# Optimization experiments

Hardware: AMD Instinct MI355X
Metric: run time of the kernel (lower is better)

The kernel has to match this reference:

```python
import jax, jax.numpy as jnp
import numpy as np

B, T, D, H = 16384, 48, 32, 64  # batch, num_lags, input_dim(num_features), hidden_size


def setup_inputs() -> dict:
    key = jax.random.key(0)
    ks = jax.random.split(key, 8)
    s = 1.0 / np.sqrt(H)  # torch-style uniform bound magnitude, approximated via scaled normal
    return {
        "x": jax.random.normal(ks[0], (B, T, D), dtype=jnp.float32),
        "h0": jax.random.normal(ks[1], (B, H), dtype=jnp.float32) * 0.01,
        "c0": jax.random.normal(ks[2], (B, H), dtype=jnp.float32) * 0.01,
        "W_att": jax.random.normal(ks[3], (1, 2 * H + T), dtype=jnp.float32) * 0.05,
        "b_att": jnp.zeros((1,), dtype=jnp.float32),
        "W_ih": jax.random.normal(ks[4], (4 * H, D), dtype=jnp.float32) * s,
        "W_hh": jax.random.normal(ks[5], (4 * H, H), dtype=jnp.float32) * s,
        "b_ih": jnp.zeros((4 * H,), dtype=jnp.float32),
        "b_hh": jnp.zeros((4 * H,), dtype=jnp.float32),
    }


def reference(x, h0, c0, W_att, b_att, W_ih, W_hh, b_ih, b_hh):
    # x: [B, T, D];  input-attention DA-RNN encoder with single-layer LSTM.
    Bn, Tn, Dn = x.shape
    Hn = h0.shape[-1]
    xT = jnp.transpose(x, (0, 2, 1))  # [B, D, T] full per-feature series, constant over t
    w_att = W_att[0]                   # [2H+T]

    def step(carry, xt):
        ht, ct = carry  # [B, H]
        hrep = jnp.broadcast_to(ht[:, None, :], (Bn, Dn, Hn))
        crep = jnp.broadcast_to(ct[:, None, :], (Bn, Dn, Hn))
        feat = jnp.concatenate([hrep, crep, xT], axis=2)  # [B, D, 2H+T]
        et = jnp.einsum('bdf,f->bd', feat, w_att) + b_att[0]  # [B, D]
        at = jax.nn.softmax(et, axis=1)                        # softmax over features
        wi = at * xt                                           # [B, D]
        gates = wi @ W_ih.T + b_ih + ht @ W_hh.T + b_hh        # [B, 4H]
        i_g, f_g, g_g, o_g = jnp.split(gates, 4, axis=1)
        i_g = jax.nn.sigmoid(i_g)
        f_g = jax.nn.sigmoid(f_g)
        g_g = jnp.tanh(g_g)
        o_g = jax.nn.sigmoid(o_g)
        ct2 = f_g * ct + i_g * g_g
        ht2 = o_g * jnp.tanh(ct2)
        return (ht2, ct2), (at, ht2)

    xs = jnp.transpose(x, (1, 0, 2))  # [T, B, D]
    _, (ats, hts) = jax.lax.scan(step, (h0, c0), xs)
    attention = jnp.transpose(ats, (1, 0, 2))       # [B, T, D]
    input_encoded = jnp.transpose(hts, (1, 0, 2))   # [B, T, H]
    return attention, input_encoded
```

## Files before the change

kernel.cpp:

```cpp
#include <hip/hip_runtime.h>

#define TT 48
#define DD 32
#define HH 64
#define BB 16384
#define LOG2E 1.4426950408889634f

typedef __bf16 bf16x8 __attribute__((ext_vector_type(8)));
typedef float f32x4 __attribute__((ext_vector_type(4)));

#define MFMA(a, b, c) __builtin_amdgcn_mfma_f32_16x16x32_bf16(a, b, c, 0, 0, 0)
#define BC(v) __builtin_bit_cast(bf16x8, v)

static __device__ __forceinline__ float exp2_f(float v) {
#if __has_builtin(__builtin_amdgcn_exp2f)
  return __builtin_amdgcn_exp2f(v);
#else
  return exp2f(v);
#endif
}
static __device__ __forceinline__ unsigned short bfu(float f) {
  __bf16 b = (__bf16)f;
  return __builtin_bit_cast(unsigned short, b);
}
static __device__ __forceinline__ float sigm2(float y) {
  return __builtin_amdgcn_rcpf(1.f + exp2_f(-y));
}
static __device__ __forceinline__ float tanh2(float y) {
  return fmaf(-2.f, __builtin_amdgcn_rcpf(1.f + exp2_f(y)), 1.f);
}


__global__ void prep_kernel(const float* __restrict__ W_ih, const float* __restrict__ W_hh,
                            const float* __restrict__ b_ih, const float* __restrict__ b_hh,
                            unsigned short* __restrict__ WhhL, unsigned short* __restrict__ WihL,
                            float* __restrict__ bsumL) {
  const int tid = threadIdx.x;
  const int l = tid & 63, qt = tid >> 6;
  const int rowl = l & 15, kq = (l >> 4) * 8;
  for (int mm = 0; mm < 4; ++mm) {
    const int m = qt * 4 + mm;
    const int g = m >> 2, hq = m & 3;
    const float s = (g == 2) ? 2.f * LOG2E : LOG2E;
    const int hidx = (hq >> 1) * 32 + (rowl >> 2) * 8 + (hq & 1) * 4 + (rowl & 3);
    const int orig = g * 64 + hidx;
    for (int c = 0; c < 2; ++c)
      for (int j = 0; j < 8; ++j)
        WhhL[(m * 2 + c) * 512 + l * 8 + j] = bfu(W_hh[orig * 64 + c * 32 + kq + j] * s);
    for (int j = 0; j < 8; ++j)
      WihL[m * 512 + l * 8 + j] = bfu(W_ih[orig * 32 + kq + j] * s);
    if ((l >> 4) == 0) bsumL[m * 16 + rowl] = (b_ih[orig] + b_hh[orig]) * s;
  }
}

static __device__ __forceinline__ void lstm_step(
    const int t, const float* __restrict__ xp, float* __restrict__ o0,
    float* __restrict__ opq, const float* av, float* xv,
    const f32x4 (&whhHi)[16][2], const f32x4 (&wihR)[16], const f32x4 (&biasR)[16],
    f32x4 (&creg)[4], bf16x8 (&bhIn)[2], bf16x8 (&bhOut)[2],
    const float4 av0, const float4 av1) {
  *(float4*)(o0 + t * DD) = av0;
  *(float4*)(o0 + t * DD + 4) = av1;
  bf16x8 bxw;
#pragma unroll
  for (int j = 0; j < 8; ++j) bxw[j] = (__bf16)(xv[j] * av[j]);
  const int tn = (t + 2 < TT) ? (t + 2) : (TT - 1);
  {
    const float* xnp = xp + (size_t)tn * DD;
    float4 x0 = *(const float4*)xnp, x1 = *(const float4*)(xnp + 4);
    xv[0] = x0.x; xv[1] = x0.y; xv[2] = x0.z; xv[3] = x0.w;
    xv[4] = x1.x; xv[5] = x1.y; xv[6] = x1.z; xv[7] = x1.w;
  }
#pragma unroll
  for (int hq = 0; hq < 4; ++hq) {
    f32x4 acc[4];
#pragma unroll
    for (int g = 0; g < 4; ++g) {
      const int m = g * 4 + hq;
      f32x4 A = MFMA(BC(wihR[m]), bxw, biasR[m]);
      A = MFMA(BC(whhHi[m][0]), bhIn[0], A);
      A = MFMA(BC(whhHi[m][1]), bhIn[1], A);
      acc[g] = A;
    }
    float hr[4];
#pragma unroll
    for (int r = 0; r < 4; ++r) {
      float ig = sigm2(acc[0][r]);
      float fg = sigm2(acc[1][r]);
      float gts = fmaf(-4.f * LOG2E,
                       __builtin_amdgcn_rcpf(1.f + exp2_f(acc[2][r])), 2.f * LOG2E);
      float og = sigm2(acc[3][r]);
      float cns = fmaf(fg, creg[hq][r], ig * gts);
      creg[hq][r] = cns;
      hr[r] = og * tanh2(cns);
    }
    float4 hv;
    hv.x = hr[0]; hv.y = hr[1]; hv.z = hr[2]; hv.w = hr[3];
    *(float4*)(opq + (size_t)t * HH + (hq >> 1) * 32 + (hq & 1) * 4) = hv;
#pragma unroll
    for (int r = 0; r < 4; ++r) bhOut[hq >> 1][(hq & 1) * 4 + r] = (__bf16)hr[r];
  }
}

__global__ __launch_bounds__(256, 1) void lstm_kernel(
    const float* __restrict__ x, const float* __restrict__ h0, const float* __restrict__ c0,
    const float* __restrict__ W_att, const unsigned short* __restrict__ WhhL,
    const unsigned short* __restrict__ WihL, const float* __restrict__ bsumL,
    float* __restrict__ out0, float* __restrict__ out1) {
  const int tid = threadIdx.x;
  const int l = tid & 63;
  const int wid = tid >> 6;
  const int b = l & 15;
  const int qp = l >> 4;
  const int brow = blockIdx.x * 64 + wid * 16 + b;

  f32x4 whhHi[16][2], wihR[16], biasR[16];
#pragma unroll
  for (int m = 0; m < 16; ++m) {
#pragma unroll
    for (int c = 0; c < 2; ++c)
      whhHi[m][c] = *(const f32x4*)(WhhL + ((m * 2 + c) << 9) + l * 8);
    wihR[m] = *(const f32x4*)(WihL + (m << 9) + l * 8);
    biasR[m] = *(const f32x4*)(bsumL + m * 16 + qp * 4);
  }
#pragma unroll
  for (int m = 0; m < 16; ++m) {
#pragma unroll
    for (int c = 0; c < 2; ++c) asm volatile("" : "+v"(whhHi[m][c]));
    asm volatile("" : "+a"(wihR[m]));
    asm volatile("" : "+a"(biasR[m]));
  }

  const float* xp = x + (size_t)brow * (TT * DD) + qp * 8;

  float p[8];
#pragma unroll
  for (int j = 0; j < 8; ++j) p[j] = 0.f;
#pragma unroll 4
  for (int t = 0; t < TT; ++t) {
    const float w = W_att[2 * HH + t];
    float4 x0 = *(const float4*)(xp + t * DD);
    float4 x1 = *(const float4*)(xp + t * DD + 4);
    p[0] = fmaf(x0.x, w, p[0]); p[1] = fmaf(x0.y, w, p[1]);
    p[2] = fmaf(x0.z, w, p[2]); p[3] = fmaf(x0.w, w, p[3]);
    p[4] = fmaf(x1.x, w, p[4]); p[5] = fmaf(x1.y, w, p[5]);
    p[6] = fmaf(x1.z, w, p[6]); p[7] = fmaf(x1.w, w, p[7]);
  }
  float av[8];
  {
    float mx = fmaxf(fmaxf(fmaxf(p[0], p[1]), fmaxf(p[2], p[3])),
                     fmaxf(fmaxf(p[4], p[5]), fmaxf(p[6], p[7])));
    mx = fmaxf(mx, __shfl_xor(mx, 16));
    mx = fmaxf(mx, __shfl_xor(mx, 32));
    float s = 0.f;
#pragma unroll
    for (int j = 0; j < 8; ++j) {
      av[j] = exp2_f((p[j] - mx) * LOG2E);
      s += av[j];
    }
    s += __shfl_xor(s, 16);
    s += __shfl_xor(s, 32);
    float inv = __builtin_amdgcn_rcpf(s);
#pragma unroll
    for (int j = 0; j < 8; ++j) av[j] *= inv;
  }
  float4 av0, av1;
  av0.x = av[0]; av0.y = av[1]; av0.z = av[2]; av0.w = av[3];
  av1.x = av[4]; av1.y = av[5]; av1.z = av[6]; av1.w = av[7];
  float* o0 = out0 + (size_t)brow * (TT * DD) + qp * 8;

  f32x4 creg[4];
#pragma unroll
  for (int hq = 0; hq < 4; ++hq) {
    f32x4 cv = *(const f32x4*)(c0 + (size_t)brow * HH + (hq >> 1) * 32 + qp * 8 + (hq & 1) * 4);
#pragma unroll
    for (int r = 0; r < 4; ++r) cv[r] *= 2.f * LOG2E;
    creg[hq] = cv;
  }

  bf16x8 bhA[2], bhB[2];
#pragma unroll
  for (int c = 0; c < 2; ++c) {
    const float* hp = h0 + (size_t)brow * HH + c * 32 + qp * 8;
    float4 v0 = *(const float4*)hp, v1 = *(const float4*)(hp + 4);
    float vv[8] = {v0.x, v0.y, v0.z, v0.w, v1.x, v1.y, v1.z, v1.w};
#pragma unroll
    for (int j = 0; j < 8; ++j) bhA[c][j] = (__bf16)vv[j];
  }

  float* opq = out1 + (size_t)brow * (TT * HH) + qp * 8;
  float xvA[8], xvB[8];
  {
    float4 x0 = *(const float4*)xp, x1 = *(const float4*)(xp + 4);
    xvA[0] = x0.x; xvA[1] = x0.y; xvA[2] = x0.z; xvA[3] = x0.w;
    xvA[4] = x1.x; xvA[5] = x1.y; xvA[6] = x1.z; xvA[7] = x1.w;
    float4 y0 = *(const float4*)(xp + DD), y1 = *(const float4*)(xp + DD + 4);
    xvB[0] = y0.x; xvB[1] = y0.y; xvB[2] = y0.z; xvB[3] = y0.w;
    xvB[4] = y1.x; xvB[5] = y1.y; xvB[6] = y1.z; xvB[7] = y1.w;
  }

#pragma unroll 1
  for (int t = 0; t < TT; t += 2) {
    lstm_step(t, xp, o0, opq, av, xvA, whhHi, wihR, biasR, creg, bhA, bhB, av0, av1);
    lstm_step(t + 1, xp, o0, opq, av, xvB, whhHi, wihR, biasR, creg, bhB, bhA, av0, av1);
  }
}

extern "C" void kernel_launch(void* const* d_in, const int* in_sizes, int n_in,
                              void* d_out, int out_size, void* d_ws, size_t ws_size,
                              hipStream_t stream) {
  const float* x = (const float*)d_in[0];
  const float* h0 = (const float*)d_in[1];
  const float* c0 = (const float*)d_in[2];
  const float* W_att = (const float*)d_in[3];
  const float* W_ih = (const float*)d_in[5];
  const float* W_hh = (const float*)d_in[6];
  const float* b_ih = (const float*)d_in[7];
  const float* b_hh = (const float*)d_in[8];

  float* out0 = (float*)d_out;
  float* out1 = out0 + (size_t)BB * TT * DD;

  char* ws = (char*)d_ws;
  unsigned short* WhhL = (unsigned short*)ws;
  unsigned short* WihL = (unsigned short*)(ws + 32768);
  float* bsumL = (float*)(ws + 49152);

  prep_kernel<<<1, 256, 0, stream>>>(W_ih, W_hh, b_ih, b_hh, WhhL, WihL, bsumL);
  lstm_kernel<<<BB / 64, 256, 0, stream>>>(x, h0, c0, W_att, WhhL, WihL, bsumL, out0, out1);
}
```

Before: 120.1 us.

## Interleave two independent batch tiles per wave to hide recurrence latency

```diff
diff --git a/kernel.cpp b/kernel.cpp
--- a/kernel.cpp
+++ b/kernel.cpp
@@ -102,37 +102,9 @@
   }
 }
 
-__global__ __launch_bounds__(256, 1) void lstm_kernel(
-    const float* __restrict__ x, const float* __restrict__ h0, const float* __restrict__ c0,
-    const float* __restrict__ W_att, const unsigned short* __restrict__ WhhL,
-    const unsigned short* __restrict__ WihL, const float* __restrict__ bsumL,
-    float* __restrict__ out0, float* __restrict__ out1) {
-  const int tid = threadIdx.x;
-  const int l = tid & 63;
-  const int wid = tid >> 6;
-  const int b = l & 15;
-  const int qp = l >> 4;
-  const int brow = blockIdx.x * 64 + wid * 16 + b;
-
-  f32x4 whhHi[16][2], wihR[16], biasR[16];
-#pragma unroll
-  for (int m = 0; m < 16; ++m) {
-#pragma unroll
-    for (int c = 0; c < 2; ++c)
-      whhHi[m][c] = *(const f32x4*)(WhhL + ((m * 2 + c) << 9) + l * 8);
-    wihR[m] = *(const f32x4*)(WihL + (m << 9) + l * 8);
-    biasR[m] = *(const f32x4*)(bsumL + m * 16 + qp * 4);
-  }
-#pragma unroll
-  for (int m = 0; m < 16; ++m) {
-#pragma unroll
-    for (int c = 0; c < 2; ++c) asm volatile("" : "+v"(whhHi[m][c]));
-    asm volatile("" : "+a"(wihR[m]));
-    asm volatile("" : "+a"(biasR[m]));
-  }
-
-  const float* xp = x + (size_t)brow * (TT * DD) + qp * 8;
-
+static __device__ __forceinline__ void attn_prologue(
+    const float* __restrict__ xp, const float* __restrict__ W_att,
+    float* av, float4& av0, float4& av1) {
   float p[8];
 #pragma unroll
   for (int j = 0; j < 8; ++j) p[j] = 0.f;
@@ -146,63 +118,122 @@
     p[4] = fmaf(x1.x, w, p[4]); p[5] = fmaf(x1.y, w, p[5]);
     p[6] = fmaf(x1.z, w, p[6]); p[7] = fmaf(x1.w, w, p[7]);
   }
-  float av[8];
-  {
-    float mx = fmaxf(fmaxf(fmaxf(p[0], p[1]), fmaxf(p[2], p[3])),
-                     fmaxf(fmaxf(p[4], p[5]), fmaxf(p[6], p[7])));
-    mx = fmaxf(mx, __shfl_xor(mx, 16));
-    mx = fmaxf(mx, __shfl_xor(mx, 32));
-    float s = 0.f;
-#pragma unroll
-    for (int j = 0; j < 8; ++j) {
-      av[j] = exp2_f((p[j] - mx) * LOG2E);
-      s += av[j];
-    }
-    s += __shfl_xor(s, 16);
-    s += __shfl_xor(s, 32);
-    float inv = __builtin_amdgcn_rcpf(s);
-#pragma unroll
-    for (int j = 0; j < 8; ++j) av[j] *= inv;
-  }
-  float4 av0, av1;
+  float mx = fmaxf(fmaxf(fmaxf(p[0], p[1]), fmaxf(p[2], p[3])),
+                   fmaxf(fmaxf(p[4], p[5]), fmaxf(p[6], p[7])));
+  mx = fmaxf(mx, __shfl_xor(mx, 16));
+  mx = fmaxf(mx, __shfl_xor(mx, 32));
+  float s = 0.f;
+#pragma unroll
+  for (int j = 0; j < 8; ++j) {
+    av[j] = exp2_f((p[j] - mx) * LOG2E);
+    s += av[j];
+  }
+  s += __shfl_xor(s, 16);
+  s += __shfl_xor(s, 32);
+  float inv = __builtin_amdgcn_rcpf(s);
+#pragma unroll
+  for (int j = 0; j < 8; ++j) av[j] *= inv;
   av0.x = av[0]; av0.y = av[1]; av0.z = av[2]; av0.w = av[3];
   av1.x = av[4]; av1.y = av[5]; av1.z = av[6]; av1.w = av[7];
-  float* o0 = out0 + (size_t)brow * (TT * DD) + qp * 8;
-
-  f32x4 creg[4];
+}
+
+__global__ __launch_bounds__(128, 1) void lstm_kernel(
+    const float* __restrict__ x, const float* __restrict__ h0, const float* __restrict__ c0,
+    const float* __restrict__ W_att, const unsigned short* __restrict__ WhhL,
+    const unsigned short* __restrict__ WihL, const float* __restrict__ bsumL,
+    float* __restrict__ out0, float* __restrict__ out1) {
+  const int tid = threadIdx.x;
+  const int l = tid & 63;
+  const int wid = tid >> 6;
+  const int b = l & 15;
+  const int qp = l >> 4;
+  const int wv = blockIdx.x * 2 + wid;
+  const int browA = wv * 32 + b;
+  const int browB = browA + 16;
+
+  f32x4 whhHi[16][2], wihR[16], biasR[16];
+#pragma unroll
+  for (int m = 0; m < 16; ++m) {
+#pragma unroll
+    for (int c = 0; c < 2; ++c)
+      whhHi[m][c] = *(const f32x4*)(WhhL + ((m * 2 + c) << 9) + l * 8);
+    wihR[m] = *(const f32x4*)(WihL + (m << 9) + l * 8);
+    biasR[m] = *(const f32x4*)(bsumL + m * 16 + qp * 4);
+  }
+#pragma unroll
+  for (int m = 0; m < 16; ++m) {
+#pragma unroll
+    for (int c = 0; c < 2; ++c) asm volatile("" : "+a"(whhHi[m][c]));
+    asm volatile("" : "+a"(wihR[m]));
+    asm volatile("" : "+a"(biasR[m]));
+  }
+
+  const float* xpA = x + (size_t)browA * (TT * DD) + qp * 8;
+  const float* xpB = x + (size_t)browB * (TT * DD) + qp * 8;
+
+  float avA[8], avB[8];
+  float4 avA0, avA1, avB0, avB1;
+  attn_prologue(xpA, W_att, avA, avA0, avA1);
+  attn_prologue(xpB, W_att, avB, avB0, avB1);
+  float* o0A = out0 + (size_t)browA * (TT * DD) + qp * 8;
+  float* o0B = out0 + (size_t)browB * (TT * DD) + qp * 8;
+
+  f32x4 cregA[4], cregB[4];
 #pragma unroll
   for (int hq = 0; hq < 4; ++hq) {
-    f32x4 cv = *(const f32x4*)(c0 + (size_t)brow * HH + (hq >> 1) * 32 + qp * 8 + (hq & 1) * 4);
-#pragma unroll
-    for (int r = 0; r < 4; ++r) cv[r] *= 2.f * LOG2E;
-    creg[hq] = cv;
-  }
-
-  bf16x8 bhA[2], bhB[2];
+    const int off = (hq >> 1) * 32 + qp * 8 + (hq & 1) * 4;
+    f32x4 ca = *(const f32x4*)(c0 + (size_t)browA * HH + off);
+    f32x4 cb = *(const f32x4*)(c0 + (size_t)browB * HH + off);
+#pragma unroll
+    for (int r = 0; r < 4; ++r) {
+      ca[r] *= 2.f * LOG2E;
+      cb[r] *= 2.f * LOG2E;
+    }
+    cregA[hq] = ca;
+    cregB[hq] = cb;
+  }
+
+  bf16x8 bhA0[2], bhA1[2], bhB0[2], bhB1[2];
 #pragma unroll
   for (int c = 0; c < 2; ++c) {
-    const float* hp = h0 + (size_t)brow * HH + c * 32 + qp * 8;
-    float4 v0 = *(const float4*)hp, v1 = *(const float4*)(hp + 4);
-    float vv[8] = {v0.x, v0.y, v0.z, v0.w, v1.x, v1.y, v1.z, v1.w};
-#pragma unroll
-    for (int j = 0; j < 8; ++j) bhA[c][j] = (__bf16)vv[j];
-  }
-
-  float* opq = out1 + (size_t)brow * (TT * HH) + qp * 8;
-  float xvA[8], xvB[8];
+    const float* hpA = h0 + (size_t)browA * HH + c * 32 + qp * 8;
+    const float* hpB = h0 + (size_t)browB * HH + c * 32 + qp * 8;
+    float4 a0 = *(const float4*)hpA, a1 = *(const float4*)(hpA + 4);
+    float4 b0 = *(const float4*)hpB, b1 = *(const float4*)(hpB + 4);
+    float va[8] = {a0.x, a0.y, a0.z, a0.w, a1.x, a1.y, a1.z, a1.w};
+    float vb[8] = {b0.x, b0.y, b0.z, b0.w, b1.x, b1.y, b1.z, b1.w};
+#pragma unroll
+    for (int j = 0; j < 8; ++j) {
+      bhA0[c][j] = (__bf16)va[j];
+      bhB0[c][j] = (__bf16)vb[j];
+    }
+  }
+
+  float* opqA = out1 + (size_t)browA * (TT * HH) + qp * 8;
+  float* opqB = out1 + (size_t)browB * (TT * HH) + qp * 8;
+
+  float xvA0[8], xvA1[8], xvB0[8], xvB1[8];
   {
-    float4 x0 = *(const float4*)xp, x1 = *(const float4*)(xp + 4);
-    xvA[0] = x0.x; xvA[1] = x0.y; xvA[2] = x0.z; xvA[3] = x0.w;
-    xvA[4] = x1.x; xvA[5] = x1.y; xvA[6] = x1.z; xvA[7] = x1.w;
-    float4 y0 = *(const float4*)(xp + DD), y1 = *(const float4*)(xp + DD + 4);
-    xvB[0] = y0.x; xvB[1] = y0.y; xvB[2] = y0.z; xvB[3] = y0.w;
-    xvB[4] = y1.x; xvB[5] = y1.y; xvB[6] = y1.z; xvB[7] = y1.w;
+    float4 a0 = *(const float4*)xpA, a1 = *(const float4*)(xpA + 4);
+    float4 a2 = *(const float4*)(xpA + DD), a3 = *(const float4*)(xpA + DD + 4);
+    xvA0[0] = a0.x; xvA0[1] = a0.y; xvA0[2] = a0.z; xvA0[3] = a0.w;
+    xvA0[4] = a1.x; xvA0[5] = a1.y; xvA0[6] = a1.z; xvA0[7] = a1.w;
+    xvA1[0] = a2.x; xvA1[1] = a2.y; xvA1[2] = a2.z; xvA1[3] = a2.w;
+    xvA1[4] = a3.x; xvA1[5] = a3.y; xvA1[6] = a3.z; xvA1[7] = a3.w;
+    float4 b0 = *(const float4*)xpB, b1 = *(const float4*)(xpB + 4);
+    float4 b2 = *(const float4*)(xpB + DD), b3 = *(const float4*)(xpB + DD + 4);
+    xvB0[0] = b0.x; xvB0[1] = b0.y; xvB0[2] = b0.z; xvB0[3] = b0.w;
+    xvB0[4] = b1.x; xvB0[5] = b1.y; xvB0[6] = b1.z; xvB0[7] = b1.w;
+    xvB1[0] = b2.x; xvB1[1] = b2.y; xvB1[2] = b2.z; xvB1[3] = b2.w;
+    xvB1[4] = b3.x; xvB1[5] = b3.y; xvB1[6] = b3.z; xvB1[7] = b3.w;
   }
 
 #pragma unroll 1
   for (int t = 0; t < TT; t += 2) {
-    lstm_step(t, xp, o0, opq, av, xvA, whhHi, wihR, biasR, creg, bhA, bhB, av0, av1);
-    lstm_step(t + 1, xp, o0, opq, av, xvB, whhHi, wihR, biasR, creg, bhB, bhA, av0, av1);
+    lstm_step(t, xpA, o0A, opqA, avA, xvA0, whhHi, wihR, biasR, cregA, bhA0, bhA1, avA0, avA1);
+    lstm_step(t, xpB, o0B, opqB, avB, xvB0, whhHi, wihR, biasR, cregB, bhB0, bhB1, avB0, avB1);
+    lstm_step(t + 1, xpA, o0A, opqA, avA, xvA1, whhHi, wihR, biasR, cregA, bhA1, bhA0, avA0, avA1);
+    lstm_step(t + 1, xpB, o0B, opqB, avB, xvB1, whhHi, wihR, biasR, cregB, bhB1, bhB0, avB0, avB1);
   }
 }
 
@@ -227,5 +258,5 @@
   float* bsumL = (float*)(ws + 49152);
 
   prep_kernel<<<1, 256, 0, stream>>>(W_ih, W_hh, b_ih, b_hh, WhhL, WihL, bsumL);
-  lstm_kernel<<<BB / 64, 256, 0, stream>>>(x, h0, c0, W_att, WhhL, WihL, bsumL, out0, out1);
-}
+  lstm_kernel<<<BB / 64, 128, 0, stream>>>(x, h0, c0, W_att, WhhL, WihL, bsumL, out0, out1);
+}
```

Result: slower. 245.6 us (+104.4%).
